# Performance work log

Hardware: AMD Instinct MI355X
Metric: run time of the kernel (lower is better)

## Reference

```python
import jax, jax.numpy as jnp
import numpy as np

N_NODES = 50000
N_EDGES = 800000
IN_DIM = 128
HID = 128
N_LAYERS = 3


def setup_inputs() -> dict:
    key = jax.random.key(0)
    ks = jax.random.split(key, 12)
    x = jax.random.normal(ks[0], (N_NODES, IN_DIM), dtype=jnp.float32)
    edge_index = jax.random.randint(ks[1], (2, N_EDGES), 0, N_NODES, dtype=jnp.int64)
    s = 1.0 / np.sqrt(HID)
    # per-conv 2-layer MLP weights, stacked over layers (all dims equal since in=hidden)
    W_a = jax.random.uniform(ks[2], (N_LAYERS, HID, HID), jnp.float32, -s, s)
    b_a = jax.random.uniform(ks[3], (N_LAYERS, HID), jnp.float32, -s, s)
    W_b = jax.random.uniform(ks[4], (N_LAYERS, HID, HID), jnp.float32, -s, s)
    b_b = jax.random.uniform(ks[5], (N_LAYERS, HID), jnp.float32, -s, s)
    eps = jnp.zeros((N_LAYERS,), jnp.float32)  # train_eps=True, init 0
    W_h1 = jax.random.uniform(ks[6], (HID, HID // 2), jnp.float32, -s, s)
    b_h1 = jax.random.uniform(ks[7], (HID // 2,), jnp.float32, -s, s)
    s2 = 1.0 / np.sqrt(HID // 2)
    W_h2 = jax.random.uniform(ks[8], (HID // 2, 2), jnp.float32, -s2, s2)
    b_h2 = jax.random.uniform(ks[9], (2,), jnp.float32, -s2, s2)
    return {"x": x, "edge_index": edge_index, "eps": eps, "W_a": W_a, "b_a": b_a,
            "W_b": W_b, "b_b": b_b, "W_h1": W_h1, "b_h1": b_h1, "W_h2": W_h2, "b_h2": b_h2}


def reference(x, edge_index, eps, W_a, b_a, W_b, b_b, W_h1, b_h1, W_h2, b_h2):
    # Dropout is identity in eval mode. use_residual=False, use_input_mlp=False.
    src, dst = edge_index[0], edge_index[1]
    h = x.astype(jnp.float32)
    n = h.shape[0]
    for l in range(N_LAYERS):
        # GINConv: scatter-add of neighbor (source) features into target nodes
        agg = jax.ops.segment_sum(h[src], dst, num_segments=n)  # [N, H]
        z = (1.0 + eps[l]) * h + agg
        z = jnp.maximum(z @ W_a[l] + b_a[l], 0.0) @ W_b[l] + b_b[l]
        h = jnp.maximum(z, 0.0)  # outer ReLU after conv
    hid = jnp.maximum(h @ W_h1 + b_h1, 0.0)
    return hid @ W_h2 + b_h2  # [N, 2]
```

## Files before the change

### kernel.cpp

```cpp
#include <hip/hip_runtime.h>
#include <hip/hip_bf16.h>

#define N_NODES 50000
#define N_EDGES 800000
#define HID 128

#define NB 391
#define NBLK 160
#define EPB 5000

typedef __attribute__((ext_vector_type(8))) short short8;
typedef __attribute__((ext_vector_type(4))) float f32x4;
typedef __attribute__((ext_vector_type(4))) unsigned short us4;
typedef _Float16 hv8 __attribute__((ext_vector_type(8)));
typedef _Float16 hv4 __attribute__((ext_vector_type(4)));

__device__ __forceinline__ unsigned short f2bf(float v) {
    union { float f; unsigned u; } x; x.f = v;
    unsigned r = x.u + 0x7fff + ((x.u >> 16) & 1);
    return (unsigned short)(r >> 16);
}
__device__ __forceinline__ float bf2f(unsigned short b) {
    union { unsigned u; float f; } x; x.u = ((unsigned)b) << 16;
    return x.f;
}


__global__ __launch_bounds__(256)
void hist_k(const int* __restrict__ dst, int* __restrict__ bh, int E) {
    __shared__ int h[NB];
    for (int i = threadIdx.x; i < NB; i += 256) h[i] = 0;
    __syncthreads();
    const int base = blockIdx.x * EPB;
    const int end = min(base + EPB, E);
    for (int i = base + threadIdx.x; i < end; i += 256)
        atomicAdd(&h[dst[i] >> 7], 1);
    __syncthreads();
    for (int i = threadIdx.x; i < NB; i += 256)
        bh[i * NBLK + blockIdx.x] = h[i];
}

__global__ __launch_bounds__(256)
void scanA_k(const int* __restrict__ in, int* __restrict__ bsum, int n) {
    const int t = threadIdx.x, base = blockIdx.x * 2048 + t * 8;
    int s = 0;
#pragma unroll
    for (int k = 0; k < 8; ++k) s += (base + k < n) ? in[base + k] : 0;
    __shared__ int sh[256];
    sh[t] = s;
    __syncthreads();
    for (int o = 128; o > 0; o >>= 1) {
        if (t < o) sh[t] += sh[t + o];
        __syncthreads();
    }
    if (t == 0) bsum[blockIdx.x] = sh[0];
}

__global__ __launch_bounds__(256)
void scanC_k(const int* __restrict__ in, const int* __restrict__ bsum,
             int* __restrict__ out, int n, int B) {
    const int t = threadIdx.x, base = blockIdx.x * 2048 + t * 8;
    __shared__ int blockoff;
    if (t == 0) {
        int p = 0;
        for (int i = 0; i < blockIdx.x; ++i) p += bsum[i];
        blockoff = p;
    }
    int v[8]; int s = 0;
#pragma unroll
    for (int k = 0; k < 8; ++k) { v[k] = (base + k < n) ? in[base + k] : 0; s += v[k]; }
    __shared__ int sh[256];
    sh[t] = s;
    __syncthreads();
    for (int o = 1; o < 256; o <<= 1) {
        int u = (t >= o) ? sh[t - o] : 0;
        __syncthreads();
        sh[t] += u;
        __syncthreads();
    }
    int run = ((t == 0) ? 0 : sh[t - 1]) + blockoff;
#pragma unroll
    for (int k = 0; k < 8; ++k) {
        if (base + k < n) out[base + k] = run;
        run += v[k];
    }
}

__global__ __launch_bounds__(256)
void scatter_k(const int* __restrict__ src, const int* __restrict__ dst,
               const int* __restrict__ bhs, int* __restrict__ tmp, int E) {
    __shared__ int cur[NB];
    for (int i = threadIdx.x; i < NB; i += 256) cur[i] = bhs[i * NBLK + blockIdx.x];
    __syncthreads();
    const int base = blockIdx.x * EPB;
    const int end = min(base + EPB, E);
    for (int i = base + threadIdx.x; i < end; i += 256) {
        int d = dst[i];
        int p = atomicAdd(&cur[d >> 7], 1);
        tmp[p] = (src[i] << 7) | (d & 127);
    }
}

__global__ __launch_bounds__(256)
void bucket_k(const int* __restrict__ tmp, const int* __restrict__ bhs,
              int* __restrict__ offs, int* __restrict__ csr, int E, int N) {
    const int b = blockIdx.x;
    const int t = threadIdx.x;
    __shared__ int hist[128], excl[128], cur[128];
    const int bstart = bhs[b * NBLK];
    const int bend = (b + 1 < NB) ? bhs[(b + 1) * NBLK] : E;
    if (t < 128) hist[t] = 0;
    __syncthreads();
    for (int i = bstart + t; i < bend; i += 256)
        atomicAdd(&hist[tmp[i] & 127], 1);
    __syncthreads();
    if (t < 128) excl[t] = hist[t];
    __syncthreads();
    for (int o = 1; o < 128; o <<= 1) {
        int u = (t < 128 && t >= o) ? excl[t - o] : 0;
        __syncthreads();
        if (t < 128) excl[t] += u;
        __syncthreads();
    }
    const int node0 = b * 128;
    if (t < 128) {
        int base = bstart + ((t == 0) ? 0 : excl[t - 1]);
        if (node0 + t < N) offs[node0 + t] = base;
        cur[t] = base;
    }
    if (b == 0 && t == 0) offs[N] = E;
    __syncthreads();
    for (int i = bstart + t; i < bend; i += 256) {
        int e = tmp[i];
        int p = atomicAdd(&cur[e & 127], 1);
        csr[p] = e >> 7;
    }
}

#define XB 6250
#define WB 416
__global__ __launch_bounds__(256)
void cvt_k(const float* __restrict__ x, _Float16* __restrict__ xh,
           const float* __restrict__ Wa, const float* __restrict__ Wb,
           const float* __restrict__ Wh1,
           unsigned short* __restrict__ whi, unsigned short* __restrict__ wlo) {
    if (blockIdx.x < XB) {
        int i = blockIdx.x * 256 + threadIdx.x;
        if (i < 1600000) {
            float4 v = *(const float4*)&x[i * 4];
            hv4 o;
            o.x = (_Float16)v.x; o.y = (_Float16)v.y;
            o.z = (_Float16)v.z; o.w = (_Float16)v.w;
            *(hv4*)&xh[i * 4] = o;
        }
        return;
    }
    int id = (blockIdx.x - XB) * 256 + threadIdx.x;
    float v; int dst;
    if (id < 98304) {
        int isB = (id >= 49152);
        int id2 = isB ? id - 49152 : id;
        int l = id2 >> 14, e = id2 & 16383;
        v = isB ? Wb[id2] : Wa[id2];
        int k = e >> 7, n = e & 127;
        int w = n >> 5, ct = (n >> 4) & 1, m = n & 15;
        int ks = k >> 5, quad = (k >> 3) & 3, j = k & 7;
        int within = ((w * 8 + ks * 2 + ct) * 64 + quad * 16 + m) * 8 + j;
        dst = (2 * l + isB) * 16384 + within;
    } else if (id < 106496) {
        int e = id - 98304;
        v = Wh1[e];
        int k = e >> 6, n = e & 63;
        int w = n >> 4, m = n & 15;
        int ks = k >> 5, quad = (k >> 3) & 3, j = k & 7;
        dst = 6 * 16384 + ((w * 4 + ks) * 64 + quad * 16 + m) * 8 + j;
    } else return;
    unsigned short hi = f2bf(v);
    whi[dst] = hi;
    wlo[dst] = f2bf(v - bf2f(hi));
}

__global__ __launch_bounds__(256)
void agg16_k(const _Float16* __restrict__ h_in,
             const int* __restrict__ offs, const int* __restrict__ csr,
             const float* __restrict__ eps, int layer,
             _Float16* __restrict__ z) {
    const int qw = threadIdx.x >> 4;
    const int l16 = threadIdx.x & 15;
    const int node = blockIdx.x * 16 + qw;
    if (node >= N_NODES) return;
    const hv8* __restrict__ h8 = (const hv8*)h_in;
    const float sc = 1.0f + eps[layer];
    const int beg = offs[node], end = offs[node + 1];
    float a0[8] = {0,0,0,0,0,0,0,0};
    float a1[8] = {0,0,0,0,0,0,0,0};
    int j = beg;
    for (; j + 4 <= end; j += 4) {
        int s0 = csr[j], s1 = csr[j+1], s2 = csr[j+2], s3 = csr[j+3];
        hv8 v0 = h8[(size_t)s0 * 16 + l16];
        hv8 v1 = h8[(size_t)s1 * 16 + l16];
        hv8 v2 = h8[(size_t)s2 * 16 + l16];
        hv8 v3 = h8[(size_t)s3 * 16 + l16];
#pragma unroll
        for (int e = 0; e < 8; ++e) {
            a0[e] += (float)v0[e] + (float)v2[e];
            a1[e] += (float)v1[e] + (float)v3[e];
        }
    }
    for (; j < end; ++j) {
        hv8 v = h8[(size_t)csr[j] * 16 + l16];
#pragma unroll
        for (int e = 0; e < 8; ++e) a0[e] += (float)v[e];
    }
    hv8 self = h8[(size_t)node * 16 + l16];
    hv8 o;
#pragma unroll
    for (int e = 0; e < 8; ++e)
        o[e] = (_Float16)(sc * (float)self[e] + (a0[e] + a1[e]));
    ((hv8*)z)[(size_t)node * 16 + l16] = o;
}

template <bool HEAD>
__global__ __launch_bounds__(256)
void mlp_k(const _Float16* __restrict__ z_in,
           const unsigned short* __restrict__ WAhi, const unsigned short* __restrict__ WAlo,
           const float* __restrict__ ba,
           const unsigned short* __restrict__ WBhi, const unsigned short* __restrict__ WBlo,
           const float* __restrict__ bb,
           const unsigned short* __restrict__ WHhi, const unsigned short* __restrict__ WHlo,
           const float* __restrict__ bh1,
           const float* __restrict__ W2, const float* __restrict__ b2,
           void* __restrict__ outp) {
    __shared__ unsigned short Zhi[64 * 136];
    __shared__ unsigned short Zlo[64 * 136];
    const int t = threadIdx.x;
    const int wave = t >> 6, lane = t & 63;
    const int m = lane & 15, quad = lane >> 4;
    const int row0 = blockIdx.x * 64;

    {
        const int quart = lane >> 4, l16 = lane & 15;
        const hv8* __restrict__ z8 = (const hv8*)z_in;
        for (int g = 0; g < 4; ++g) {
            const int r = wave * 16 + g * 4 + quart;
            const int node = row0 + r;
            float o[8] = {0,0,0,0,0,0,0,0};
            if (node < N_NODES) {
                hv8 v = z8[(size_t)node * 16 + l16];
#pragma unroll
                for (int e = 0; e < 8; ++e) o[e] = (float)v[e];
            }
            us4 hi0, hi1, lo0, lo1;
#pragma unroll
            for (int e = 0; e < 4; ++e) {
                hi0[e] = f2bf(o[e]);     lo0[e] = f2bf(o[e]     - bf2f(hi0[e]));
                hi1[e] = f2bf(o[e + 4]); lo1[e] = f2bf(o[e + 4] - bf2f(hi1[e]));
            }
            *(us4*)&Zhi[r * 136 + l16 * 8]     = hi0;
            *(us4*)&Zhi[r * 136 + l16 * 8 + 4] = hi1;
            *(us4*)&Zlo[r * 136 + l16 * 8]     = lo0;
            *(us4*)&Zlo[r * 136 + l16 * 8 + 4] = lo1;
        }
    }
    __syncthreads();

    f32x4 acc[4][2];
    for (int s = 0; s < 4; ++s)
        for (int ct = 0; ct < 2; ++ct) acc[s][ct] = (f32x4){0, 0, 0, 0};
#pragma unroll 1
    for (int ks = 0; ks < 4; ++ks) {
        const int fA = (wave * 8 + ks * 2) * 512 + lane * 8;
        short8 wh0 = *(const short8*)&WAhi[fA];
        short8 wl0 = *(const short8*)&WAlo[fA];
        short8 wh1 = *(const short8*)&WAhi[fA + 512];
        short8 wl1 = *(const short8*)&WAlo[fA + 512];
        const int wo = ks * 32 + quad * 8;
#pragma unroll
        for (int s = 0; s < 4; ++s) {
            const int r = s * 16 + m;
            short8 zh = *(const short8*)&Zhi[r * 136 + wo];
            short8 zl = *(const short8*)&Zlo[r * 136 + wo];
            acc[s][0] = __builtin_amdgcn_mfma_f32_16x16x32_bf16(zh, wh0, acc[s][0], 0, 0, 0);
            acc[s][0] = __builtin_amdgcn_mfma_f32_16x16x32_bf16(zh, wl0, acc[s][0], 0, 0, 0);
            acc[s][0] = __builtin_amdgcn_mfma_f32_16x16x32_bf16(zl, wh0, acc[s][0], 0, 0, 0);
            acc[s][1] = __builtin_amdgcn_mfma_f32_16x16x32_bf16(zh, wh1, acc[s][1], 0, 0, 0);
            acc[s][1] = __builtin_amdgcn_mfma_f32_16x16x32_bf16(zh, wl1, acc[s][1], 0, 0, 0);
            acc[s][1] = __builtin_amdgcn_mfma_f32_16x16x32_bf16(zl, wh1, acc[s][1], 0, 0, 0);
        }
    }
    __syncthreads();

    for (int s = 0; s < 4; ++s) {
        for (int ct = 0; ct < 2; ++ct) {
            int c = wave * 32 + ct * 16 + m;
            float bac = ba[c];
            for (int i = 0; i < 4; ++i) {
                int r = s * 16 + quad * 4 + i;
                float v = fmaxf(acc[s][ct][i] + bac, 0.0f);
                unsigned short hv = f2bf(v);
                Zhi[r * 136 + c] = hv;
                Zlo[r * 136 + c] = f2bf(v - bf2f(hv));
            }
        }
    }
    __syncthreads();

    for (int s = 0; s < 4; ++s)
        for (int ct = 0; ct < 2; ++ct) acc[s][ct] = (f32x4){0, 0, 0, 0};
#pragma unroll 1
    for (int ks = 0; ks < 4; ++ks) {
        const int fB = (wave * 8 + ks * 2) * 512 + lane * 8;
        short8 wh0 = *(const short8*)&WBhi[fB];
        short8 wl0 = *(const short8*)&WBlo[fB];
        short8 wh1 = *(const short8*)&WBhi[fB + 512];
        short8 wl1 = *(const short8*)&WBlo[fB + 512];
        const int wo = ks * 32 + quad * 8;
#pragma unroll
        for (int s = 0; s < 4; ++s) {
            const int r = s * 16 + m;
            short8 zh = *(const short8*)&Zhi[r * 136 + wo];
            short8 zl = *(const short8*)&Zlo[r * 136 + wo];
            acc[s][0] = __builtin_amdgcn_mfma_f32_16x16x32_bf16(zh, wh0, acc[s][0], 0, 0, 0);
            acc[s][0] = __builtin_amdgcn_mfma_f32_16x16x32_bf16(zh, wl0, acc[s][0], 0, 0, 0);
            acc[s][0] = __builtin_amdgcn_mfma_f32_16x16x32_bf16(zl, wh0, acc[s][0], 0, 0, 0);
            acc[s][1] = __builtin_amdgcn_mfma_f32_16x16x32_bf16(zh, wh1, acc[s][1], 0, 0, 0);
            acc[s][1] = __builtin_amdgcn_mfma_f32_16x16x32_bf16(zh, wl1, acc[s][1], 0, 0, 0);
            acc[s][1] = __builtin_amdgcn_mfma_f32_16x16x32_bf16(zl, wh1, acc[s][1], 0, 0, 0);
        }
    }

    if (!HEAD) {
        _Float16* hout = (_Float16*)outp;
        for (int s = 0; s < 4; ++s) {
            for (int ct = 0; ct < 2; ++ct) {
                int c = wave * 32 + ct * 16 + m;
                float bbc = bb[c];
                for (int i = 0; i < 4; ++i) {
                    int row = row0 + s * 16 + quad * 4 + i;
                    if (row < N_NODES)
                        hout[(size_t)row * 128 + c] = (_Float16)fmaxf(acc[s][ct][i] + bbc, 0.0f);
                }
            }
        }
    } else {
        __syncthreads();

        for (int s = 0; s < 4; ++s) {
            for (int ct = 0; ct < 2; ++ct) {
                int c = wave * 32 + ct * 16 + m;
                float bbc = bb[c];
                for (int i = 0; i < 4; ++i) {
                    int r = s * 16 + quad * 4 + i;
                    float v = fmaxf(acc[s][ct][i] + bbc, 0.0f);
                    unsigned short hv = f2bf(v);
                    Zhi[r * 136 + c] = hv;
                    Zlo[r * 136 + c] = f2bf(v - bf2f(hv));
                }
            }
        }
        __syncthreads();

        f32x4 a3[4];
        for (int s = 0; s < 4; ++s) a3[s] = (f32x4){0, 0, 0, 0};
#pragma unroll 1
        for (int ks = 0; ks < 4; ++ks) {
            const int fH = (wave * 4 + ks) * 512 + lane * 8;
            short8 hh = *(const short8*)&WHhi[fH];
            short8 hl = *(const short8*)&WHlo[fH];
            const int wo = ks * 32 + quad * 8;
#pragma unroll
            for (int s = 0; s < 4; ++s) {
                const int r = s * 16 + m;
                short8 zh = *(const short8*)&Zhi[r * 136 + wo];
                short8 zl = *(const short8*)&Zlo[r * 136 + wo];
                a3[s] = __builtin_amdgcn_mfma_f32_16x16x32_bf16(zh, hh, a3[s], 0, 0, 0);
                a3[s] = __builtin_amdgcn_mfma_f32_16x16x32_bf16(zh, hl, a3[s], 0, 0, 0);
                a3[s] = __builtin_amdgcn_mfma_f32_16x16x32_bf16(zl, hh, a3[s], 0, 0, 0);
            }
        }
        __syncthreads();

        float* Hid = (float*)Zhi;
        for (int s = 0; s < 4; ++s) {
            int c = wave * 16 + m;
            float bc = bh1[c];
            for (int i = 0; i < 4; ++i) {
                int r = s * 16 + quad * 4 + i;
                Hid[r * 68 + c] = fmaxf(a3[s][i] + bc, 0.0f);
            }
        }
        __syncthreads();

        float* Red = (float*)Zlo;
        {
            int pair = t >> 1, seg = t & 1;
            int r = pair >> 1, col = pair & 1;
            float p = 0.0f;
#pragma unroll
            for (int j = seg * 32; j < seg * 32 + 32; ++j)
                p += Hid[r * 68 + j] * W2[j * 2 + col];
            Red[t] = p;
        }
        __syncthreads();
        if (t < 128) {
            float* outF = (float*)outp;
            int r = t >> 1, col = t & 1;
            float a = b2[col] + (Red[t * 2] + Red[t * 2 + 1]);
            int node = row0 + r;
            if (node < N_NODES) outF[(size_t)node * 2 + col] = a;
        }
    }
}


extern "C" void kernel_launch(void* const* d_in, const int* in_sizes, int n_in,
                              void* d_out, int out_size, void* d_ws, size_t ws_size,
                              hipStream_t stream) {
    const float* x    = (const float*)d_in[0];
    const int*   ei   = (const int*)d_in[1];
    const float* eps  = (const float*)d_in[2];
    const float* W_a  = (const float*)d_in[3];
    const float* b_a  = (const float*)d_in[4];
    const float* W_b  = (const float*)d_in[5];
    const float* b_b  = (const float*)d_in[6];
    const float* W_h1 = (const float*)d_in[7];
    const float* b_h1 = (const float*)d_in[8];
    const float* W_h2 = (const float*)d_in[9];
    const float* b_h2 = (const float*)d_in[10];
    float* out = (float*)d_out;

    const int N = N_NODES, E = N_EDGES;
    const int* src = ei;
    const int* dst = ei + E;

    char* ws = (char*)d_ws;
    size_t off = 0;
    auto carve = [&](size_t bytes) {
        char* p = ws + off;
        off = (off + bytes + 255) & ~(size_t)255;
        return p;
    };
    _Float16* xh   = (_Float16*)carve((size_t)N * HID * sizeof(_Float16));
    _Float16* zb   = (_Float16*)carve((size_t)N * HID * sizeof(_Float16));
    _Float16* bufA = (_Float16*)carve((size_t)N * HID * sizeof(_Float16));
    _Float16* bufB = (_Float16*)carve((size_t)N * HID * sizeof(_Float16));
    int*   tmp    = (int*)carve((size_t)E * sizeof(int));
    int*   csr    = (int*)carve((size_t)E * sizeof(int));
    int*   offs   = (int*)carve((size_t)(N + 1) * sizeof(int));
    int*   bh     = (int*)carve((size_t)NB * NBLK * sizeof(int));
    int*   bhs    = (int*)carve((size_t)NB * NBLK * sizeof(int));
    int*   bsum   = (int*)carve(64 * sizeof(int));
    unsigned short* whi = (unsigned short*)carve(7 * 16384 * sizeof(unsigned short));
    unsigned short* wlo = (unsigned short*)carve(7 * 16384 * sizeof(unsigned short));
    (void)ws_size;

    const int M = NB * NBLK;
    const int SB = (M + 2047) / 2048;
    hist_k<<<NBLK, 256, 0, stream>>>(dst, bh, E);
    scanA_k<<<SB, 256, 0, stream>>>(bh, bsum, M);
    scanC_k<<<SB, 256, 0, stream>>>(bh, bsum, bhs, M, SB);
    scatter_k<<<NBLK, 256, 0, stream>>>(src, dst, bhs, tmp, E);
    bucket_k<<<NB, 256, 0, stream>>>(tmp, bhs, offs, csr, E, N);

    cvt_k<<<XB + WB, 256, 0, stream>>>(x, xh, W_a, W_b, W_h1, whi, wlo);

    const int agg_grid = (N + 15) / 16;
    const int mlp_grid = (N + 63) / 64;
    #define WSLOT(s) (whi + (s) * 16384), (wlo + (s) * 16384)
    #define NOHEAD (const unsigned short*)nullptr, (const unsigned short*)nullptr, \
                   (const float*)nullptr, (const float*)nullptr, (const float*)nullptr

    agg16_k<<<agg_grid, 256, 0, stream>>>(xh, offs, csr, eps, 0, zb);
    mlp_k<false><<<mlp_grid, 256, 0, stream>>>(zb, WSLOT(0), b_a + 0 * 128,
        WSLOT(1), b_b + 0 * 128, NOHEAD, (void*)bufA);
    agg16_k<<<agg_grid, 256, 0, stream>>>(bufA, offs, csr, eps, 1, zb);
    mlp_k<false><<<mlp_grid, 256, 0, stream>>>(zb, WSLOT(2), b_a + 1 * 128,
        WSLOT(3), b_b + 1 * 128, NOHEAD, (void*)bufB);
    agg16_k<<<agg_grid, 256, 0, stream>>>(bufB, offs, csr, eps, 2, zb);
    mlp_k<true><<<mlp_grid, 256, 0, stream>>>(zb, WSLOT(4), b_a + 2 * 128,
        WSLOT(5), b_b + 2 * 128, WSLOT(6), b_h1, W_h2, b_h2, (void*)out);
}
```

Baseline: 275.8 us.

## Fuse CSR build and conversion into one cooperative kernel; coalesce MLP output stores

Replaces the six preprocessing launches (histogram, two scan passes, scatter, bucket sort, fp16/bf16 conversion) with one 160-block cooperative kernel that separates phases with grid.sync(). The scan is restructured to run per block over contiguous chunks of the histogram. Separately, the non-head MLP epilogue now stages its outputs through shared memory and writes full 16-byte rows instead of scattered 2-byte stores. The trade-off is that the preprocessing runs on only 160 blocks with several grid barriers, so conversion and bucketing have less parallelism than before.

```diff
diff --git a/kernel.cpp b/kernel.cpp
--- a/kernel.cpp
+++ b/kernel.cpp
@@ -1,5 +1,8 @@
 #include <hip/hip_runtime.h>
 #include <hip/hip_bf16.h>
+#include <hip/hip_cooperative_groups.h>
+
+namespace cg = cooperative_groups;
 
 #define N_NODES 50000
 #define N_EDGES 800000
@@ -25,159 +28,158 @@
     return x.f;
 }
 
-
 __global__ __launch_bounds__(256)
-void hist_k(const int* __restrict__ dst, int* __restrict__ bh, int E) {
-    __shared__ int h[NB];
-    for (int i = threadIdx.x; i < NB; i += 256) h[i] = 0;
-    __syncthreads();
-    const int base = blockIdx.x * EPB;
-    const int end = min(base + EPB, E);
-    for (int i = base + threadIdx.x; i < end; i += 256)
-        atomicAdd(&h[dst[i] >> 7], 1);
-    __syncthreads();
-    for (int i = threadIdx.x; i < NB; i += 256)
-        bh[i * NBLK + blockIdx.x] = h[i];
-}
-
-__global__ __launch_bounds__(256)
-void scanA_k(const int* __restrict__ in, int* __restrict__ bsum, int n) {
-    const int t = threadIdx.x, base = blockIdx.x * 2048 + t * 8;
-    int s = 0;
-#pragma unroll
-    for (int k = 0; k < 8; ++k) s += (base + k < n) ? in[base + k] : 0;
-    __shared__ int sh[256];
-    sh[t] = s;
-    __syncthreads();
-    for (int o = 128; o > 0; o >>= 1) {
-        if (t < o) sh[t] += sh[t + o];
-        __syncthreads();
-    }
-    if (t == 0) bsum[blockIdx.x] = sh[0];
-}
-
-__global__ __launch_bounds__(256)
-void scanC_k(const int* __restrict__ in, const int* __restrict__ bsum,
-             int* __restrict__ out, int n, int B) {
-    const int t = threadIdx.x, base = blockIdx.x * 2048 + t * 8;
-    __shared__ int blockoff;
-    if (t == 0) {
-        int p = 0;
-        for (int i = 0; i < blockIdx.x; ++i) p += bsum[i];
-        blockoff = p;
-    }
-    int v[8]; int s = 0;
-#pragma unroll
-    for (int k = 0; k < 8; ++k) { v[k] = (base + k < n) ? in[base + k] : 0; s += v[k]; }
-    __shared__ int sh[256];
-    sh[t] = s;
-    __syncthreads();
-    for (int o = 1; o < 256; o <<= 1) {
-        int u = (t >= o) ? sh[t - o] : 0;
-        __syncthreads();
-        sh[t] += u;
-        __syncthreads();
-    }
-    int run = ((t == 0) ? 0 : sh[t - 1]) + blockoff;
-#pragma unroll
-    for (int k = 0; k < 8; ++k) {
-        if (base + k < n) out[base + k] = run;
-        run += v[k];
-    }
-}
-
-__global__ __launch_bounds__(256)
-void scatter_k(const int* __restrict__ src, const int* __restrict__ dst,
-               const int* __restrict__ bhs, int* __restrict__ tmp, int E) {
-    __shared__ int cur[NB];
-    for (int i = threadIdx.x; i < NB; i += 256) cur[i] = bhs[i * NBLK + blockIdx.x];
-    __syncthreads();
-    const int base = blockIdx.x * EPB;
-    const int end = min(base + EPB, E);
-    for (int i = base + threadIdx.x; i < end; i += 256) {
-        int d = dst[i];
-        int p = atomicAdd(&cur[d >> 7], 1);
-        tmp[p] = (src[i] << 7) | (d & 127);
-    }
-}
-
-__global__ __launch_bounds__(256)
-void bucket_k(const int* __restrict__ tmp, const int* __restrict__ bhs,
-              int* __restrict__ offs, int* __restrict__ csr, int E, int N) {
-    const int b = blockIdx.x;
-    const int t = threadIdx.x;
+void build_k(const int* __restrict__ src, const int* __restrict__ dst,
+             int* __restrict__ bh, int* __restrict__ gsum, int* __restrict__ bhs,
+             int* __restrict__ tmp, int* __restrict__ offs, int* __restrict__ csr,
+             const float* __restrict__ x, _Float16* __restrict__ xh,
+             const float* __restrict__ Wa, const float* __restrict__ Wb,
+             const float* __restrict__ Wh1,
+             unsigned short* __restrict__ whi, unsigned short* __restrict__ wlo) {
+    cg::grid_group grid = cg::this_grid();
+    const int blk = blockIdx.x, t = threadIdx.x;
+    __shared__ int sh[NB];
+    __shared__ int red[256];
     __shared__ int hist[128], excl[128], cur[128];
-    const int bstart = bhs[b * NBLK];
-    const int bend = (b + 1 < NB) ? bhs[(b + 1) * NBLK] : E;
-    if (t < 128) hist[t] = 0;
-    __syncthreads();
-    for (int i = bstart + t; i < bend; i += 256)
-        atomicAdd(&hist[tmp[i] & 127], 1);
-    __syncthreads();
-    if (t < 128) excl[t] = hist[t];
-    __syncthreads();
-    for (int o = 1; o < 128; o <<= 1) {
-        int u = (t < 128 && t >= o) ? excl[t - o] : 0;
-        __syncthreads();
-        if (t < 128) excl[t] += u;
-        __syncthreads();
-    }
-    const int node0 = b * 128;
-    if (t < 128) {
-        int base = bstart + ((t == 0) ? 0 : excl[t - 1]);
-        if (node0 + t < N) offs[node0 + t] = base;
-        cur[t] = base;
-    }
-    if (b == 0 && t == 0) offs[N] = E;
-    __syncthreads();
-    for (int i = bstart + t; i < bend; i += 256) {
-        int e = tmp[i];
-        int p = atomicAdd(&cur[e & 127], 1);
-        csr[p] = e >> 7;
-    }
-}
-
-#define XB 6250
-#define WB 416
-__global__ __launch_bounds__(256)
-void cvt_k(const float* __restrict__ x, _Float16* __restrict__ xh,
-           const float* __restrict__ Wa, const float* __restrict__ Wb,
-           const float* __restrict__ Wh1,
-           unsigned short* __restrict__ whi, unsigned short* __restrict__ wlo) {
-    if (blockIdx.x < XB) {
-        int i = blockIdx.x * 256 + threadIdx.x;
-        if (i < 1600000) {
+
+    for (int i = t; i < NB; i += 256) sh[i] = 0;
+    __syncthreads();
+    {
+        const int base = blk * EPB;
+        for (int i = base + t; i < base + EPB; i += 256)
+            atomicAdd(&sh[dst[i] >> 7], 1);
+    }
+    __syncthreads();
+    for (int i = t; i < NB; i += 256) bh[i * NBLK + blk] = sh[i];
+
+    {
+        const int base = blk * 10000;
+        for (int q = t; q < 10000; q += 256) {
+            int i = base + q;
             float4 v = *(const float4*)&x[i * 4];
             hv4 o;
             o.x = (_Float16)v.x; o.y = (_Float16)v.y;
             o.z = (_Float16)v.z; o.w = (_Float16)v.w;
             *(hv4*)&xh[i * 4] = o;
         }
-        return;
-    }
-    int id = (blockIdx.x - XB) * 256 + threadIdx.x;
-    float v; int dst;
-    if (id < 98304) {
-        int isB = (id >= 49152);
-        int id2 = isB ? id - 49152 : id;
-        int l = id2 >> 14, e = id2 & 16383;
-        v = isB ? Wb[id2] : Wa[id2];
-        int k = e >> 7, n = e & 127;
-        int w = n >> 5, ct = (n >> 4) & 1, m = n & 15;
-        int ks = k >> 5, quad = (k >> 3) & 3, j = k & 7;
-        int within = ((w * 8 + ks * 2 + ct) * 64 + quad * 16 + m) * 8 + j;
-        dst = (2 * l + isB) * 16384 + within;
-    } else if (id < 106496) {
-        int e = id - 98304;
-        v = Wh1[e];
-        int k = e >> 6, n = e & 63;
-        int w = n >> 4, m = n & 15;
-        int ks = k >> 5, quad = (k >> 3) & 3, j = k & 7;
-        dst = 6 * 16384 + ((w * 4 + ks) * 64 + quad * 16 + m) * 8 + j;
-    } else return;
-    unsigned short hi = f2bf(v);
-    whi[dst] = hi;
-    wlo[dst] = f2bf(v - bf2f(hi));
+        for (int q = t; q < 666; q += 256) {
+            int id = blk * 666 + q;
+            float v; int dsti;
+            if (id < 98304) {
+                int isB = (id >= 49152);
+                int id2 = isB ? id - 49152 : id;
+                int l = id2 >> 14, e = id2 & 16383;
+                v = isB ? Wb[id2] : Wa[id2];
+                int k = e >> 7, n = e & 127;
+                int w = n >> 5, ct = (n >> 4) & 1, m = n & 15;
+                int ks = k >> 5, quad = (k >> 3) & 3, j = k & 7;
+                dsti = (2 * l + isB) * 16384 +
+                       ((w * 8 + ks * 2 + ct) * 64 + quad * 16 + m) * 8 + j;
+            } else if (id < 106496) {
+                int e = id - 98304;
+                v = Wh1[e];
+                int k = e >> 6, n = e & 63;
+                int w = n >> 4, m = n & 15;
+                int ks = k >> 5, quad = (k >> 3) & 3, j = k & 7;
+                dsti = 6 * 16384 + ((w * 4 + ks) * 64 + quad * 16 + m) * 8 + j;
+            } else continue;
+            unsigned short hi = f2bf(v);
+            whi[dsti] = hi;
+            wlo[dsti] = f2bf(v - bf2f(hi));
+        }
+    }
+    grid.sync();
+
+    {
+        const int base = blk * 391;
+        int s = 0;
+        for (int i = t; i < 391; i += 256) s += bh[base + i];
+        red[t] = s;
+        __syncthreads();
+        for (int o = 128; o > 0; o >>= 1) {
+            if (t < o) red[t] += red[t + o];
+            __syncthreads();
+        }
+        if (t == 0) gsum[blk] = red[0];
+    }
+    grid.sync();
+
+    if (blk == 0) {
+        int v = (t < NBLK) ? gsum[t] : 0;
+        red[t] = v;
+        __syncthreads();
+        for (int o = 1; o < 256; o <<= 1) {
+            int u = (t >= o) ? red[t - o] : 0;
+            __syncthreads();
+            red[t] += u;
+            __syncthreads();
+        }
+        if (t < NBLK) gsum[t] = red[t] - v;
+    }
+    grid.sync();
+
+    {
+        const int base = blk * 391;
+        int i0 = t * 2, i1 = t * 2 + 1;
+        int v0 = (i0 < 391) ? bh[base + i0] : 0;
+        int v1 = (i1 < 391) ? bh[base + i1] : 0;
+        red[t] = v0 + v1;
+        __syncthreads();
+        for (int o = 1; o < 256; o <<= 1) {
+            int u = (t >= o) ? red[t - o] : 0;
+            __syncthreads();
+            red[t] += u;
+            __syncthreads();
+        }
+        int ex = ((t == 0) ? 0 : red[t - 1]) + gsum[blk];
+        if (i0 < 391) bhs[base + i0] = ex;
+        if (i1 < 391) bhs[base + i1] = ex + v0;
+    }
+    grid.sync();
+
+    for (int i = t; i < NB; i += 256) sh[i] = bhs[i * NBLK + blk];
+    __syncthreads();
+    {
+        const int base = blk * EPB;
+        for (int i = base + t; i < base + EPB; i += 256) {
+            int d = dst[i];
+            int p = atomicAdd(&sh[d >> 7], 1);
+            tmp[p] = (src[i] << 7) | (d & 127);
+        }
+    }
+    grid.sync();
+
+    if (blk == 0 && t == 0) offs[N_NODES] = N_EDGES;
+    for (int b = blk; b < NB; b += NBLK) {
+        const int bstart = bhs[b * NBLK];
+        const int bend = (b + 1 < NB) ? bhs[(b + 1) * NBLK] : N_EDGES;
+        if (t < 128) hist[t] = 0;
+        __syncthreads();
+        for (int i = bstart + t; i < bend; i += 256)
+            atomicAdd(&hist[tmp[i] & 127], 1);
+        __syncthreads();
+        if (t < 128) excl[t] = hist[t];
+        __syncthreads();
+        for (int o = 1; o < 128; o <<= 1) {
+            int u = (t < 128 && t >= o) ? excl[t - o] : 0;
+            __syncthreads();
+            if (t < 128) excl[t] += u;
+            __syncthreads();
+        }
+        const int node0 = b * 128;
+        if (t < 128) {
+            int base = bstart + ((t == 0) ? 0 : excl[t - 1]);
+            if (node0 + t < N_NODES) offs[node0 + t] = base;
+            cur[t] = base;
+        }
+        __syncthreads();
+        for (int i = bstart + t; i < bend; i += 256) {
+            int e = tmp[i];
+            int p = atomicAdd(&cur[e & 127], 1);
+            csr[p] = e >> 7;
+        }
+        __syncthreads();
+    }
 }
 
 __global__ __launch_bounds__(256)
@@ -330,16 +332,27 @@
     }
 
     if (!HEAD) {
-        _Float16* hout = (_Float16*)outp;
+        __syncthreads();
+        _Float16* Uh = (_Float16*)Zhi;
         for (int s = 0; s < 4; ++s) {
             for (int ct = 0; ct < 2; ++ct) {
                 int c = wave * 32 + ct * 16 + m;
                 float bbc = bb[c];
                 for (int i = 0; i < 4; ++i) {
-                    int row = row0 + s * 16 + quad * 4 + i;
-                    if (row < N_NODES)
-                        hout[(size_t)row * 128 + c] = (_Float16)fmaxf(acc[s][ct][i] + bbc, 0.0f);
+                    int r = s * 16 + quad * 4 + i;
+                    Uh[r * 136 + c] = (_Float16)fmaxf(acc[s][ct][i] + bbc, 0.0f);
                 }
+            }
+        }
+        __syncthreads();
+        _Float16* hout = (_Float16*)outp;
+        const int quart = lane >> 4, l16 = lane & 15;
+        for (int g = 0; g < 4; ++g) {
+            int r = wave * 16 + g * 4 + quart;
+            int node = row0 + r;
+            if (node < N_NODES) {
+                hv8 v = *(hv8*)&Uh[r * 136 + l16 * 8];
+                ((hv8*)hout)[(size_t)node * 16 + l16] = v;
             }
         }
     } else {
@@ -449,20 +462,19 @@
     int*   offs   = (int*)carve((size_t)(N + 1) * sizeof(int));
     int*   bh     = (int*)carve((size_t)NB * NBLK * sizeof(int));
     int*   bhs    = (int*)carve((size_t)NB * NBLK * sizeof(int));
-    int*   bsum   = (int*)carve(64 * sizeof(int));
+    int*   gsum   = (int*)carve(256 * sizeof(int));
     unsigned short* whi = (unsigned short*)carve(7 * 16384 * sizeof(unsigned short));
     unsigned short* wlo = (unsigned short*)carve(7 * 16384 * sizeof(unsigned short));
     (void)ws_size;
 
-    const int M = NB * NBLK;
-    const int SB = (M + 2047) / 2048;
-    hist_k<<<NBLK, 256, 0, stream>>>(dst, bh, E);
-    scanA_k<<<SB, 256, 0, stream>>>(bh, bsum, M);
-    scanC_k<<<SB, 256, 0, stream>>>(bh, bsum, bhs, M, SB);
-    scatter_k<<<NBLK, 256, 0, stream>>>(src, dst, bhs, tmp, E);
-    bucket_k<<<NB, 256, 0, stream>>>(tmp, bhs, offs, csr, E, N);
-
-    cvt_k<<<XB + WB, 256, 0, stream>>>(x, xh, W_a, W_b, W_h1, whi, wlo);
+    {
+        void* bargs[] = {(void*)&src, (void*)&dst, (void*)&bh, (void*)&gsum,
+                         (void*)&bhs, (void*)&tmp, (void*)&offs, (void*)&csr,
+                         (void*)&x, (void*)&xh, (void*)&W_a, (void*)&W_b,
+                         (void*)&W_h1, (void*)&whi, (void*)&wlo};
+        hipLaunchCooperativeKernel((void*)build_k, dim3(NBLK), dim3(256),
+                                   bargs, 0, stream);
+    }
 
     const int agg_grid = (N + 15) / 16;
     const int mlp_grid = (N + 63) / 64;
```

Measured after the change: 405.0 us. +46.9%, slower.
